# Kernel optimization log

Hardware: AMD Instinct MI355X
Metric: run time of the kernel (lower is better)

Reference implementation:

```python
import jax, jax.numpy as jnp
import numpy as np

PARAM = 10.0
EPS = 1e-10

def delu(x):
    # delu_feature_map: param*relu(x) + (exp(param*min(x,0)) - 1) + 1
    return PARAM * jax.nn.relu(x) + jnp.expm1(PARAM * jnp.minimum(x, 0.0)) + 1.0

def conv1x1(x, w, b):
    # x: (B,C,H,W), w: (O,C), b: (O,)
    return jnp.einsum('oc,bchw->bohw', w, x) + b[None, :, None, None]

def conv3x3(x, w, b):
    # x: (B,C,H,W), w: (O,C,3,3)
    y = jax.lax.conv_general_dilated(x, w, window_strides=(1, 1), padding='SAME',
                                     dimension_numbers=('NCHW', 'OIHW', 'NCHW'))
    return y + b[None, :, None, None]

def setup_inputs() -> dict:
    key = jax.random.key(0)
    B, C, H, W = 4, 256, 128, 128
    ks = jax.random.split(key, 20)
    s = 0.05
    d = {
        'x1': jax.random.normal(ks[0], (B, C, H, W), jnp.float32),
        'x2': jax.random.normal(ks[1], (B, C, H, W), jnp.float32),
        'wq1': jax.random.normal(ks[2], (C, C), jnp.float32) * s,
        'bq1': jax.random.normal(ks[3], (C,), jnp.float32) * s,
        'wk1': jax.random.normal(ks[4], (C, C), jnp.float32) * s,
        'bk1': jax.random.normal(ks[5], (C,), jnp.float32) * s,
        'wv1': jax.random.normal(ks[6], (C, C), jnp.float32) * s,
        'bv1': jax.random.normal(ks[7], (C,), jnp.float32) * s,
        'wq2': jax.random.normal(ks[8], (C, C), jnp.float32) * s,
        'bq2': jax.random.normal(ks[9], (C,), jnp.float32) * s,
        'wk2': jax.random.normal(ks[10], (C, C), jnp.float32) * s,
        'bk2': jax.random.normal(ks[11], (C,), jnp.float32) * s,
        'wv2': jax.random.normal(ks[12], (C, C), jnp.float32) * s,
        'bv2': jax.random.normal(ks[13], (C,), jnp.float32) * s,
        'wd1': jax.random.normal(ks[14], (C, C), jnp.float32) * s,
        'bd1': jax.random.normal(ks[15], (C,), jnp.float32) * s,
        'wd3': jax.random.normal(ks[16], (C, C, 3, 3), jnp.float32) * s,
        'bd3': jax.random.normal(ks[17], (C,), jnp.float32) * s,
        'gamma1': jax.random.normal(ks[18], (1,), jnp.float32) * 0.5,
        'gamma2': jax.random.normal(ks[19], (1,), jnp.float32) * 0.5,
    }
    return d

def reference(x1, x2, wq1, bq1, wk1, bk1, wv1, bv1, wq2, bq2, wk2, bk2,
              wv2, bv2, wd1, bd1, wd3, bd3, gamma1, gamma2):
    B, C, H, W = x1.shape
    N = H * W
    # QKV projections (1x1 convs), flattened to (B,C,N). delu is elementwise,
    # so applying it on (B,C,N) equals the permute/delu/permute in torch.
    q1 = delu(conv1x1(x1, wq1, bq1).reshape(B, C, N))
    k1 = delu(conv1x1(x1, wk1, bk1).reshape(B, C, N))
    v1 = conv1x1(x1, wv1, bv1).reshape(B, C, N)
    q2 = delu(conv1x1(x2, wq2, bq2).reshape(B, C, N))
    k2 = delu(conv1x1(x2, wk2, bk2).reshape(B, C, N))
    v2 = conv1x1(x2, wv2, bv2).reshape(B, C, N)

    # energy: (B,C,C) cross-kernel matrices
    energy1 = jnp.einsum('bmn,bcn->bmc', q1, k2)
    energy2 = jnp.einsum('bmn,bcn->bmc', q2, k1)

    KV1 = k1 * v1  # (B,C,N)
    KV2 = k2 * v2

    # norm: 1 / (sum_{m,c} energy[b,m,c] * k[b,c,n] + eps) -> (B,N)
    esum1 = energy1.sum(axis=1)  # (B,C)
    esum2 = energy2.sum(axis=1)
    norm1 = 1.0 / (jnp.einsum('bc,bcn->bn', esum1, k2) + EPS)
    norm2 = 1.0 / (jnp.einsum('bc,bcn->bn', esum2, k1) + EPS)

    # einsum('bmc,bcn,bn->bcn') factorizes: sum over m hits only energy
    att1 = (esum1[:, :, None] * KV1 * norm1[:, None, :]).reshape(B, C, H, W)
    att2 = (esum2[:, :, None] * KV2 * norm2[:, None, :]).reshape(B, C, H, W)

    out1 = att1 + conv1x1(x1, wd1, bd1) + conv3x3(x1, wd3, bd3)
    out2 = att2 + conv1x1(x2, wd1, bd1) + conv3x3(x2, wd3, bd3)
    out1 = x1 + gamma1[0] * out1
    out2 = x2 + gamma2[0] * out2
    return (out1, out2)
```

## Files before the change

kernel.cpp:

```cpp
#include <hip/hip_runtime.h>
#include <stdint.h>

#define Bn 4
#define Cn 256
#define Hn 128
#define Wn 128
#define Nn 16384
#define EPSn 1e-10f

typedef unsigned short u16;
typedef __attribute__((ext_vector_type(8))) short short8;
typedef __attribute__((ext_vector_type(4))) short short4v;
typedef __attribute__((ext_vector_type(4))) float f32x4;

#define GLOAD_LDS16(g, l)                                                        \
    __builtin_amdgcn_global_load_lds(                                            \
        (const __attribute__((address_space(1))) unsigned int*)(const void*)(g), \
        (__attribute__((address_space(3))) unsigned int*)(void*)(l), 16, 0, 0)

#define MFMA16(a, b, c) __builtin_amdgcn_mfma_f32_16x16x32_bf16(a, b, c, 0, 0, 0)

__device__ __forceinline__ float bf2f(u16 u) {
    union { float f; uint32_t i; } v; v.i = ((uint32_t)u) << 16; return v.f;
}
__device__ __forceinline__ u16 f2bf(float f) {
    union { float f; uint32_t i; } v; v.f = f;
    uint32_t r = v.i + 0x7FFFu + ((v.i >> 16) & 1u);
    return (u16)(r >> 16);
}
__device__ __forceinline__ float delu_f(float x) {
    return x >= 0.f ? fmaf(10.f, x, 1.f) : __expf(10.f * x);
}

__global__ void prep_kernel(const float* __restrict__ wq1, const float* __restrict__ wk1,
                            const float* __restrict__ wv1,
                            const float* __restrict__ wq2, const float* __restrict__ wk2,
                            const float* __restrict__ wv2,
                            const float* __restrict__ wd1, const float* __restrict__ wd3,
                            const float* __restrict__ bd1, const float* __restrict__ bd3,
                            const float* __restrict__ gamma1, const float* __restrict__ gamma2,
                            u16* __restrict__ wq1p, u16* __restrict__ wk1p, u16* __restrict__ wv1p,
                            u16* __restrict__ wq2p, u16* __restrict__ wk2p, u16* __restrict__ wv2p,
                            u16* __restrict__ wallp1, u16* __restrict__ wallp2,
                            float* __restrict__ bfused)
{
    int idx = blockIdx.x * 256 + threadIdx.x;
    int o = idx >> 8, c = idx & 255;
    if (idx < 256) bfused[idx] = bd1[idx] + bd3[idx];
    int s = o >> 6, mf = (o >> 4) & 3, lr = o & 15;
    int kc = c >> 5, lk = (c >> 3) & 3, j = c & 7;
    int poff = ((kc * 4 + s) * 4 + mf) * 512 + (lk * 16 + lr) * 8 + j;
    wq1p[poff] = f2bf(wq1[idx]);
    wk1p[poff] = f2bf(wk1[idx]);
    wv1p[poff] = f2bf(wv1[idx]);
    wq2p[poff] = f2bf(wq2[idx]);
    wk2p[poff] = f2bf(wk2[idx]);
    wv2p[poff] = f2bf(wv2[idx]);
    float wd1v = wd1[idx];
    float inv1 = 1.f / gamma1[0];
    float inv2 = 1.f / gamma2[0];
    float diag = (o == c) ? 1.f : 0.f;
    #pragma unroll
    for (int tap = 0; tap < 9; ++tap) {
        float w = wd3[idx * 9 + tap] + (tap == 4 ? wd1v : 0.f);
        wallp1[tap * 65536 + poff] = f2bf(w + (tap == 4 ? diag * inv1 : 0.f));
        wallp2[tap * 65536 + poff] = f2bf(w + (tap == 4 ? diag * inv2 : 0.f));
    }
}

__global__ void transpose_kernel(const float* __restrict__ x1, const float* __restrict__ x2,
                                 u16* __restrict__ xT1, u16* __restrict__ xT2)
{
    __shared__ __align__(16) u16 tl[64][72];
    int t = threadIdx.x;
    int z = blockIdx.z, img = z >> 2, b = z & 3;
    const float* x = img ? x2 : x1;
    u16* xT = img ? xT2 : xT1;
    int n0 = blockIdx.x * 64, c0 = blockIdx.y * 64;
    int cl = t >> 4, nl = (t & 15) * 4;
    #pragma unroll
    for (int pc = 0; pc < 4; ++pc) {
        int c = pc * 16 + cl;
        float4 v = *(const float4*)&x[((size_t)(b * Cn + c0 + c)) * Nn + n0 + nl];
        tl[nl + 0][c] = f2bf(v.x);
        tl[nl + 1][c] = f2bf(v.y);
        tl[nl + 2][c] = f2bf(v.z);
        tl[nl + 3][c] = f2bf(v.w);
    }
    __syncthreads();
    #pragma unroll
    for (int ps = 0; ps < 2; ++ps) {
        int id = ps * 256 + t;
        int nr = id >> 3, cc = (id & 7) * 8;
        short8 v = *(const short8*)&tl[nr][cc];
        *(short8*)&xT[((size_t)(b * Nn + n0 + nr)) * 256 + c0 + cc] = v;
    }
}

__global__ __launch_bounds__(256, 2) void qkv_kernel(
    const u16* __restrict__ xT1, const u16* __restrict__ xT2,
    const u16* __restrict__ wq1p, const u16* __restrict__ wk1p, const u16* __restrict__ wv1p,
    const u16* __restrict__ wq2p, const u16* __restrict__ wk2p, const u16* __restrict__ wv2p,
    const float* __restrict__ bq1, const float* __restrict__ bk1, const float* __restrict__ bv1,
    const float* __restrict__ bq2, const float* __restrict__ bk2, const float* __restrict__ bv2,
    u16* __restrict__ k1, u16* __restrict__ k2,
    u16* __restrict__ kv1, u16* __restrict__ kv2,
    float* __restrict__ qsum1, float* __restrict__ qsum2)
{
    __shared__ __align__(16) u16 Bt[2 * 4096];
    int t = threadIdx.x;
    int nb = blockIdx.x, mb = blockIdx.y;
    int z = blockIdx.z, img = z >> 2, b = z & 3;
    const u16* xT  = img ? xT2  : xT1;
    const u16* wqp = img ? wq2p : wq1p;
    const u16* wkp = img ? wk2p : wk1p;
    const u16* wvp = img ? wv2p : wv1p;
    const float* bq = img ? bq2 : bq1;
    const float* bk = img ? bk2 : bk1;
    const float* bv = img ? bv2 : bv1;
    u16* kout  = img ? k2  : k1;
    u16* kvout = img ? kv2 : kv1;
    float* qsum = img ? qsum2 : qsum1;

    int lane = t & 63, wid = t >> 6;
    int wm = wid >> 1, wn = wid & 1;
    int lr = lane & 15, lk = lane >> 4;
    int s = mb * 2 + wm;

    f32x4 zf = {0.f, 0.f, 0.f, 0.f};
    f32x4 accq[4][4], acck[4][4], accv[4][4];
    #pragma unroll
    for (int i = 0; i < 4; ++i)
        #pragma unroll
        for (int j = 0; j < 4; ++j) { accq[i][j] = zf; acck[i][j] = zf; accv[i][j] = zf; }

    int colp = lane >> 2, chp = (lane & 3) * 8;
    auto STAGE = [&](int bufi, int kc) {
        #pragma unroll
        for (int i = 0; i < 2; ++i) {
            int col0 = (wid * 2 + i) * 16;
            const u16* g = xT + ((size_t)(b * Nn + nb * 128 + col0 + colp)) * 256 + kc * 32 + chp;
            GLOAD_LDS16(g, &Bt[bufi * 4096 + col0 * 32]);
        }
    };

    STAGE(0, 0);
    __syncthreads();

    for (int kc = 0; kc < 8; ++kc) {
        int cur = kc & 1;
        if (kc < 7) STAGE(cur ^ 1, kc + 1);
        int abase = ((kc * 4 + s) * 4) * 512 + lane * 8;
        short8 bf[4];
        #pragma unroll
        for (int nf = 0; nf < 4; ++nf)
            bf[nf] = *(const short8*)&Bt[cur * 4096 + (wn * 64 + nf * 16 + lr) * 32 + lk * 8];
        #pragma unroll
        for (int mf = 0; mf < 4; ++mf) {
            short8 aq = *(const short8*)&wqp[abase + mf * 512];
            short8 ak = *(const short8*)&wkp[abase + mf * 512];
            short8 av = *(const short8*)&wvp[abase + mf * 512];
            __builtin_amdgcn_s_setprio(1);
            #pragma unroll
            for (int nf = 0; nf < 4; ++nf) {
                accq[mf][nf] = MFMA16(aq, bf[nf], accq[mf][nf]);
                acck[mf][nf] = MFMA16(ak, bf[nf], acck[mf][nf]);
                accv[mf][nf] = MFMA16(av, bf[nf], accv[mf][nf]);
            }
            __builtin_amdgcn_s_setprio(0);
        }
        __syncthreads();
    }

    float qs[4] = {0.f, 0.f, 0.f, 0.f};
    #pragma unroll
    for (int mf = 0; mf < 4; ++mf) {
        #pragma unroll
        for (int r = 0; r < 4; ++r) {
            int o = mb * 128 + wm * 64 + mf * 16 + lk * 4 + r;
            float bqv = bq[o], bkv = bk[o], bvv = bv[o];
            #pragma unroll
            for (int nf = 0; nf < 4; ++nf) {
                int n = nb * 128 + wn * 64 + nf * 16 + lr;
                size_t idx = ((size_t)(b * Cn + o)) * Nn + n;
                float qv = delu_f(accq[mf][nf][r] + bqv);
                qs[nf] += qv;
                float kk = delu_f(acck[mf][nf][r] + bkv);
                kout[idx] = f2bf(kk);
                float vv = accv[mf][nf][r] + bvv;
                kvout[idx] = f2bf(kk * vv);
            }
        }
    }
    #pragma unroll
    for (int nf = 0; nf < 4; ++nf) {
        float sgl = qs[nf];
        sgl += __shfl_xor(sgl, 16);
        sgl += __shfl_xor(sgl, 32);
        if (lk == 0)
            atomicAdd(&qsum[b * Nn + nb * 128 + wn * 64 + nf * 16 + lr], sgl);
    }
}

__global__ void esum_kernel(const u16* __restrict__ k1, const u16* __restrict__ k2,
                            const float* __restrict__ qsum1, const float* __restrict__ qsum2,
                            float* __restrict__ esum1, float* __restrict__ esum2)
{
    int c = blockIdx.x, b = blockIdx.y, pair = blockIdx.z, t = threadIdx.x;
    const u16* k = pair ? k1 : k2;
    const float* qsum = pair ? qsum2 : qsum1;
    float* esum = pair ? esum2 : esum1;
    const u16* kr = k + ((size_t)(b * Cn + c)) * Nn;
    const float* qr = qsum + b * Nn;
    float s = 0.f;
    for (int i = t * 8; i < Nn; i += 2048) {
        short8 kv = *(const short8*)&kr[i];
        #pragma unroll
        for (int j = 0; j < 8; ++j) s = fmaf(bf2f((u16)kv[j]), qr[i + j], s);
    }
    #pragma unroll
    for (int m = 32; m; m >>= 1) s += __shfl_xor(s, m);
    __shared__ float red[4];
    if ((t & 63) == 0) red[t >> 6] = s;
    __syncthreads();
    if (t == 0) esum[b * Cn + c] = red[0] + red[1] + red[2] + red[3];
}

__global__ void norm_kernel(const u16* __restrict__ k1, const u16* __restrict__ k2,
                            const float* __restrict__ esum1, const float* __restrict__ esum2,
                            float* __restrict__ norm1, float* __restrict__ norm2)
{
    __shared__ float es[256];
    int t = threadIdx.x, b = blockIdx.y, pair = blockIdx.z;
    const u16* k = pair ? k1 : k2;
    const float* esum = pair ? esum2 : esum1;
    float* nrm = pair ? norm2 : norm1;
    es[t] = esum[b * Cn + t];
    __syncthreads();
    int n = blockIdx.x * 256 + t;
    const u16* kb = k + (size_t)b * Cn * Nn + n;
    float a = 0.f;
    #pragma unroll 8
    for (int c = 0; c < 256; ++c)
        a = fmaf(es[c], bf2f(kb[(size_t)c * Nn]), a);
    nrm[b * Nn + n] = 1.f / (a + EPSn);
}

#define BSZ6 (6 * 130 * 32)

__global__ __launch_bounds__(512, 2) void conv_att_kernel(
    const u16* __restrict__ xT,
    const u16* __restrict__ wallp, const float* __restrict__ bfused,
    const u16* __restrict__ kv, const float* __restrict__ esum,
    const float* __restrict__ nrm, const float* __restrict__ gamma,
    float* __restrict__ out)
{
    __shared__ __align__(16) u16 Bl[2 * BSZ6];
    int t = threadIdx.x;
    int lin = (blockIdx.z * 32 + blockIdx.y) * 2 + blockIdx.x;
    int mb = lin & 1, b = (lin >> 1) & 3, ys = lin >> 3;
    int ybase = ys * 4;
    int lane = t & 63, wid = t >> 6;
    int wm = wid & 1, wy = wid >> 1;
    int lr = lane & 15, lk = lane >> 4;
    int s = mb * 2 + wm;

    f32x4 zf = {0.f, 0.f, 0.f, 0.f};
    f32x4 acc[4][8];
    #pragma unroll
    for (int i = 0; i < 4; ++i)
        #pragma unroll
        for (int j = 0; j < 8; ++j) acc[i][j] = zf;

    if (t < 96) {
        int buf = t / 48, r = t % 48;
        int row = r >> 3, pos = ((r >> 2) & 1) ? 129 : 0, q = r & 3;
        short8 z = {0, 0, 0, 0, 0, 0, 0, 0};
        *(short8*)&Bl[buf * BSZ6 + (row * 130 + pos) * 32 + q * 8] = z;
    }

    int colp = lane >> 2, chp = (lane & 3) * 8;
    auto STAGE = [&](int bufi, int kc) {
        #pragma unroll
        for (int i = 0; i < 6; ++i) {
            int run = wid * 6 + i;
            int hy = run >> 3, sx = run & 7;
            int yy = ybase + hy - 1;
            int dst = bufi * BSZ6 + (hy * 130 + 1 + sx * 16) * 32;
            if (yy < 0 || yy >= Hn) {
                short8 z = {0, 0, 0, 0, 0, 0, 0, 0};
                *(short8*)&Bl[dst + lane * 8] = z;
            } else {
                const u16* g = xT + ((size_t)(b * Nn + yy * Wn + sx * 16 + colp)) * 256
                                  + kc * 32 + chp;
                GLOAD_LDS16(g, &Bl[dst]);
            }
        }
    };

    STAGE(0, 0);
    __syncthreads();

    for (int kc = 0; kc < 8; ++kc) {
        int cur = kc & 1;
        int abase = ((kc * 4 + s) * 4) * 512 + lane * 8;
        short8 af[3][4];
        #pragma unroll
        for (int mf = 0; mf < 4; ++mf)
            af[0][mf] = *(const short8*)&wallp[0 * 65536 + abase + mf * 512];
        #pragma unroll
        for (int mf = 0; mf < 4; ++mf)
            af[1][mf] = *(const short8*)&wallp[1 * 65536 + abase + mf * 512];
        if (kc < 7) STAGE(cur ^ 1, kc + 1);
        int cb = cur * BSZ6;
        #pragma unroll
        for (int tap = 0; tap < 9; ++tap) {
            if (tap < 7) {
                #pragma unroll
                for (int mf = 0; mf < 4; ++mf)
                    af[(tap + 2) % 3][mf] =
                        *(const short8*)&wallp[(tap + 2) * 65536 + abase + mf * 512];
            }
            int dy = tap / 3, dx = tap % 3;
            short8 bf[8];
            #pragma unroll
            for (int nf = 0; nf < 8; ++nf)
                bf[nf] = *(const short8*)&Bl[cb + ((wy + dy) * 130 + nf * 16 + lr + dx) * 32 + lk * 8];
            __builtin_amdgcn_s_setprio(1);
            #pragma unroll
            for (int mf = 0; mf < 4; ++mf) {
                #pragma unroll
                for (int nf = 0; nf < 8; ++nf)
                    acc[mf][nf] = MFMA16(af[tap % 3][mf], bf[nf], acc[mf][nf]);
            }
            __builtin_amdgcn_s_setprio(0);
        }
        __syncthreads();
    }

    float g = gamma[0];
    int y = ybase + wy;
    int nbase = y * Wn;
    float nr8[8];
    #pragma unroll
    for (int nf = 0; nf < 8; ++nf)
        nr8[nf] = nrm[b * Nn + nbase + nf * 16 + lr];
    #pragma unroll
    for (int mf = 0; mf < 4; ++mf) {
        #pragma unroll
        for (int r = 0; r < 4; ++r) {
            int o = mb * 128 + wm * 64 + mf * 16 + lk * 4 + r;
            float es_o = esum[b * Cn + o];
            float bf_o = bfused[o];
            size_t rowbase = ((size_t)(b * Cn + o)) * Nn + nbase;
            #pragma unroll
            for (int nf = 0; nf < 8; ++nf) {
                size_t idx = rowbase + nf * 16 + lr;
                float att = es_o * bf2f(kv[idx]) * nr8[nf];
                out[idx] = g * (acc[mf][nf][r] + bf_o + att);
            }
        }
    }
}

extern "C" void kernel_launch(void* const* d_in, const int* in_sizes, int n_in,
                              void* d_out, int out_size, void* d_ws, size_t ws_size,
                              hipStream_t stream)
{
    const float* x1  = (const float*)d_in[0];
    const float* x2  = (const float*)d_in[1];
    const float* wq1 = (const float*)d_in[2];
    const float* bq1 = (const float*)d_in[3];
    const float* wk1 = (const float*)d_in[4];
    const float* bk1 = (const float*)d_in[5];
    const float* wv1 = (const float*)d_in[6];
    const float* bv1 = (const float*)d_in[7];
    const float* wq2 = (const float*)d_in[8];
    const float* bq2 = (const float*)d_in[9];
    const float* wk2 = (const float*)d_in[10];
    const float* bk2 = (const float*)d_in[11];
    const float* wv2 = (const float*)d_in[12];
    const float* bv2 = (const float*)d_in[13];
    const float* wd1 = (const float*)d_in[14];
    const float* bd1 = (const float*)d_in[15];
    const float* wd3 = (const float*)d_in[16];
    const float* bd3 = (const float*)d_in[17];
    const float* gamma1 = (const float*)d_in[18];
    const float* gamma2 = (const float*)d_in[19];

    char* ws = (char*)d_ws;
    size_t off = 0;
    auto alloc = [&](size_t bytes) { char* p = ws + off; off += (bytes + 255) & ~(size_t)255; return p; };

    u16* xT1    = (u16*)alloc((size_t)Bn * Nn * Cn * 2);
    u16* xT2    = (u16*)alloc((size_t)Bn * Nn * Cn * 2);
    u16* k1     = (u16*)alloc((size_t)Bn * Cn * Nn * 2);
    u16* k2     = (u16*)alloc((size_t)Bn * Cn * Nn * 2);
    u16* kv2    = (u16*)alloc((size_t)Bn * Cn * Nn * 2);
    u16* wallp1 = (u16*)alloc((size_t)9 * 65536 * 2);
    u16* wallp2 = (u16*)alloc((size_t)9 * 65536 * 2);
    u16* wq1p   = (u16*)alloc(65536 * 2);
    u16* wk1p   = (u16*)alloc(65536 * 2);
    u16* wv1p   = (u16*)alloc(65536 * 2);
    u16* wq2p   = (u16*)alloc(65536 * 2);
    u16* wk2p   = (u16*)alloc(65536 * 2);
    u16* wv2p   = (u16*)alloc(65536 * 2);
    float* qsum1 = (float*)alloc(Bn * Nn * 4);
    float* qsum2 = (float*)alloc(Bn * Nn * 4);
    float* esum1 = (float*)alloc(Bn * Cn * 4);
    float* esum2 = (float*)alloc(Bn * Cn * 4);
    float* norm1 = (float*)alloc(Bn * Nn * 4);
    float* norm2 = (float*)alloc(Bn * Nn * 4);
    float* bfused = (float*)alloc(Cn * 4);

    float* out1 = (float*)d_out;
    float* out2 = out1 + (size_t)Bn * Cn * Nn;
    u16* kv1 = (u16*)out2;

    hipMemsetAsync(qsum1, 0, Bn * Nn * 4, stream);
    hipMemsetAsync(qsum2, 0, Bn * Nn * 4, stream);

    prep_kernel<<<dim3(256), dim3(256), 0, stream>>>(wq1, wk1, wv1, wq2, wk2, wv2, wd1, wd3,
                                                     bd1, bd3, gamma1, gamma2,
                                                     wq1p, wk1p, wv1p, wq2p, wk2p, wv2p,
                                                     wallp1, wallp2, bfused);
    transpose_kernel<<<dim3(256, 4, 8), 256, 0, stream>>>(x1, x2, xT1, xT2);
    qkv_kernel<<<dim3(128, 2, 8), 256, 0, stream>>>(xT1, xT2,
                                                    wq1p, wk1p, wv1p, wq2p, wk2p, wv2p,
                                                    bq1, bk1, bv1, bq2, bk2, bv2,
                                                    k1, k2, kv1, kv2, qsum1, qsum2);
    esum_kernel<<<dim3(256, 4, 2), 256, 0, stream>>>(k1, k2, qsum1, qsum2, esum1, esum2);
    norm_kernel<<<dim3(64, 4, 2), 256, 0, stream>>>(k1, k2, esum1, esum2, norm1, norm2);
    conv_att_kernel<<<dim3(2, 32, 4), 512, 0, stream>>>(xT1, wallp1, bfused, kv1,
                                                        esum1, norm1, gamma1, out1);
    conv_att_kernel<<<dim3(2, 32, 4), 512, 0, stream>>>(xT2, wallp2, bfused, kv2,
                                                        esum2, norm2, gamma2, out2);
}
```

Measured before the change: 357.2 us.

## Shrink QKV tile, stage outputs through LDS, remap conv blocks per XCD

The QKV kernel now works on 64-column tiles instead of 128, halving accumulator registers so the launch bound can allow three blocks per CU, and the grid doubles to match. The k and k*v outputs are written into an LDS buffer first and then stored as coalesced 16-byte vectors, replacing scattered 2-byte global stores. The conv_att block index is also remapped so blocks of the same batch and neighbouring row strips land on the same XCD, which should improve L2 locality. The costs are extra LDS traffic and barriers, and smaller tiles mean the weight fragments are reloaded more often per output.

New measurement: 354.2 us. No clear change (-0.9%).

```diff
diff --git a/kernel.cpp b/kernel.cpp
--- a/kernel.cpp
+++ b/kernel.cpp
@@ -97,7 +97,7 @@
     }
 }
 
-__global__ __launch_bounds__(256, 2) void qkv_kernel(
+__global__ __launch_bounds__(256, 3) void qkv_kernel(
     const u16* __restrict__ xT1, const u16* __restrict__ xT2,
     const u16* __restrict__ wq1p, const u16* __restrict__ wk1p, const u16* __restrict__ wv1p,
     const u16* __restrict__ wq2p, const u16* __restrict__ wk2p, const u16* __restrict__ wv2p,
@@ -107,7 +107,8 @@
     u16* __restrict__ kv1, u16* __restrict__ kv2,
     float* __restrict__ qsum1, float* __restrict__ qsum2)
 {
-    __shared__ __align__(16) u16 Bt[2 * 4096];
+    __shared__ __align__(16) u16 Bt[2 * 2048];
+    __shared__ __align__(16) u16 obuf[128 * 64];
     int t = threadIdx.x;
     int nb = blockIdx.x, mb = blockIdx.y;
     int z = blockIdx.z, img = z >> 2, b = z & 3;
@@ -122,26 +123,23 @@
     u16* kvout = img ? kv2 : kv1;
     float* qsum = img ? qsum2 : qsum1;
 
+    int n0 = nb * 64;
     int lane = t & 63, wid = t >> 6;
     int wm = wid >> 1, wn = wid & 1;
     int lr = lane & 15, lk = lane >> 4;
     int s = mb * 2 + wm;
 
     f32x4 zf = {0.f, 0.f, 0.f, 0.f};
-    f32x4 accq[4][4], acck[4][4], accv[4][4];
+    f32x4 accq[4][2], acck[4][2], accv[4][2];
     #pragma unroll
     for (int i = 0; i < 4; ++i)
         #pragma unroll
-        for (int j = 0; j < 4; ++j) { accq[i][j] = zf; acck[i][j] = zf; accv[i][j] = zf; }
+        for (int j = 0; j < 2; ++j) { accq[i][j] = zf; acck[i][j] = zf; accv[i][j] = zf; }
 
     int colp = lane >> 2, chp = (lane & 3) * 8;
     auto STAGE = [&](int bufi, int kc) {
-        #pragma unroll
-        for (int i = 0; i < 2; ++i) {
-            int col0 = (wid * 2 + i) * 16;
-            const u16* g = xT + ((size_t)(b * Nn + nb * 128 + col0 + colp)) * 256 + kc * 32 + chp;
-            GLOAD_LDS16(g, &Bt[bufi * 4096 + col0 * 32]);
-        }
+        const u16* g = xT + ((size_t)(b * Nn + n0 + wid * 16 + colp)) * 256 + kc * 32 + chp;
+        GLOAD_LDS16(g, &Bt[bufi * 2048 + (wid * 16) * 32]);
     };
 
     STAGE(0, 0);
@@ -151,10 +149,10 @@
         int cur = kc & 1;
         if (kc < 7) STAGE(cur ^ 1, kc + 1);
         int abase = ((kc * 4 + s) * 4) * 512 + lane * 8;
-        short8 bf[4];
-        #pragma unroll
-        for (int nf = 0; nf < 4; ++nf)
-            bf[nf] = *(const short8*)&Bt[cur * 4096 + (wn * 64 + nf * 16 + lr) * 32 + lk * 8];
+        short8 bf[2];
+        #pragma unroll
+        for (int nf = 0; nf < 2; ++nf)
+            bf[nf] = *(const short8*)&Bt[cur * 2048 + (wn * 32 + nf * 16 + lr) * 32 + lk * 8];
         #pragma unroll
         for (int mf = 0; mf < 4; ++mf) {
             short8 aq = *(const short8*)&wqp[abase + mf * 512];
@@ -162,7 +160,7 @@
             short8 av = *(const short8*)&wvp[abase + mf * 512];
             __builtin_amdgcn_s_setprio(1);
             #pragma unroll
-            for (int nf = 0; nf < 4; ++nf) {
+            for (int nf = 0; nf < 2; ++nf) {
                 accq[mf][nf] = MFMA16(aq, bf[nf], accq[mf][nf]);
                 acck[mf][nf] = MFMA16(ak, bf[nf], acck[mf][nf]);
                 accv[mf][nf] = MFMA16(av, bf[nf], accv[mf][nf]);
@@ -172,33 +170,70 @@
         __syncthreads();
     }
 
-    float qs[4] = {0.f, 0.f, 0.f, 0.f};
+    float qs[2] = {0.f, 0.f};
     #pragma unroll
     for (int mf = 0; mf < 4; ++mf) {
         #pragma unroll
         for (int r = 0; r < 4; ++r) {
             int o = mb * 128 + wm * 64 + mf * 16 + lk * 4 + r;
-            float bqv = bq[o], bkv = bk[o], bvv = bv[o];
-            #pragma unroll
-            for (int nf = 0; nf < 4; ++nf) {
-                int n = nb * 128 + wn * 64 + nf * 16 + lr;
-                size_t idx = ((size_t)(b * Cn + o)) * Nn + n;
-                float qv = delu_f(accq[mf][nf][r] + bqv);
-                qs[nf] += qv;
-                float kk = delu_f(acck[mf][nf][r] + bkv);
-                kout[idx] = f2bf(kk);
-                float vv = accv[mf][nf][r] + bvv;
-                kvout[idx] = f2bf(kk * vv);
-            }
-        }
-    }
-    #pragma unroll
-    for (int nf = 0; nf < 4; ++nf) {
+            float bqv = bq[o];
+            #pragma unroll
+            for (int nf = 0; nf < 2; ++nf)
+                qs[nf] += delu_f(accq[mf][nf][r] + bqv);
+        }
+    }
+    #pragma unroll
+    for (int nf = 0; nf < 2; ++nf) {
         float sgl = qs[nf];
         sgl += __shfl_xor(sgl, 16);
         sgl += __shfl_xor(sgl, 32);
         if (lk == 0)
-            atomicAdd(&qsum[b * Nn + nb * 128 + wn * 64 + nf * 16 + lr], sgl);
+            atomicAdd(&qsum[b * Nn + n0 + wn * 32 + nf * 16 + lr], sgl);
+    }
+
+    #pragma unroll
+    for (int mf = 0; mf < 4; ++mf) {
+        #pragma unroll
+        for (int r = 0; r < 4; ++r) {
+            int ol = wm * 64 + mf * 16 + lk * 4 + r;
+            float bkv = bk[mb * 128 + ol];
+            #pragma unroll
+            for (int nf = 0; nf < 2; ++nf)
+                obuf[ol * 64 + wn * 32 + nf * 16 + lr] = f2bf(delu_f(acck[mf][nf][r] + bkv));
+        }
+    }
+    __syncthreads();
+    #pragma unroll
+    for (int i = 0; i < 4; ++i) {
+        int sid = t * 4 + i;
+        int o = sid >> 3, seg = sid & 7;
+        short8 v = *(const short8*)&obuf[o * 64 + seg * 8];
+        *(short8*)&kout[((size_t)(b * Cn + mb * 128 + o)) * Nn + n0 + seg * 8] = v;
+    }
+    __syncthreads();
+
+    #pragma unroll
+    for (int mf = 0; mf < 4; ++mf) {
+        #pragma unroll
+        for (int r = 0; r < 4; ++r) {
+            int ol = wm * 64 + mf * 16 + lk * 4 + r;
+            float bkv = bk[mb * 128 + ol];
+            float bvv = bv[mb * 128 + ol];
+            #pragma unroll
+            for (int nf = 0; nf < 2; ++nf) {
+                float kk = delu_f(acck[mf][nf][r] + bkv);
+                float vv = accv[mf][nf][r] + bvv;
+                obuf[ol * 64 + wn * 32 + nf * 16 + lr] = f2bf(kk * vv);
+            }
+        }
+    }
+    __syncthreads();
+    #pragma unroll
+    for (int i = 0; i < 4; ++i) {
+        int sid = t * 4 + i;
+        int o = sid >> 3, seg = sid & 7;
+        short8 v = *(const short8*)&obuf[o * 64 + seg * 8];
+        *(short8*)&kvout[((size_t)(b * Cn + mb * 128 + o)) * Nn + n0 + seg * 8] = v;
     }
 }
 
@@ -258,7 +293,10 @@
     __shared__ __align__(16) u16 Bl[2 * BSZ6];
     int t = threadIdx.x;
     int lin = (blockIdx.z * 32 + blockIdx.y) * 2 + blockIdx.x;
-    int mb = lin & 1, b = (lin >> 1) & 3, ys = lin >> 3;
+    int xcd = lin & 7, slot = lin >> 3;
+    int b = xcd >> 1;
+    int ys = (xcd & 1) * 16 + (slot >> 1);
+    int mb = slot & 1;
     int ybase = ys * 4;
     int lane = t & 63, wid = t >> 6;
     int wm = wid & 1, wy = wid >> 1;
@@ -425,7 +463,7 @@
                                                      wq1p, wk1p, wv1p, wq2p, wk2p, wv2p,
                                                      wallp1, wallp2, bfused);
     transpose_kernel<<<dim3(256, 4, 8), 256, 0, stream>>>(x1, x2, xT1, xT2);
-    qkv_kernel<<<dim3(128, 2, 8), 256, 0, stream>>>(xT1, xT2,
+    qkv_kernel<<<dim3(256, 2, 8), 256, 0, stream>>>(xT1, xT2,
                                                     wq1p, wk1p, wv1p, wq2p, wk2p, wv2p,
                                                     bq1, bk1, bv1, bq2, bk2, bv2,
                                                     k1, k2, kv1, kv2, qsum1, qsum2);
```
